# Kernel optimization log

Measured on AMD Instinct MI355X. Metric: run time of the kernel, lower is better.

## Reference

```python
import jax, jax.numpy as jnp
import numpy as np
import math

D_MODEL = 1024
NUM_HEADS = 16
D_KV = 64
INNER = NUM_HEADS * D_KV
NUM_BUCKETS = 32
MAX_DISTANCE = 128


def _relative_position_bucket(relative_position, num_buckets=NUM_BUCKETS, max_distance=MAX_DISTANCE):
    # bidirectional T5 bucketing
    n = -relative_position
    num_buckets = num_buckets // 2
    ret = (n < 0).astype(jnp.int32) * num_buckets
    n = jnp.abs(n)
    max_exact = num_buckets // 2
    is_small = n < max_exact
    n_safe = jnp.maximum(n, 1).astype(jnp.float32)  # avoid log(0); masked by is_small
    val_if_large = max_exact + (
        jnp.log(n_safe / max_exact) / math.log(max_distance / max_exact) * (num_buckets - max_exact)
    ).astype(jnp.int32)
    val_if_large = jnp.minimum(val_if_large, num_buckets - 1)
    return jnp.where(is_small, n, val_if_large) + ret


def _position_bias(rel_emb, q_len, k_len):
    ctx = jnp.arange(q_len)[:, None]
    mem = jnp.arange(k_len)[None, :]
    buckets = _relative_position_bucket(mem - ctx)          # [q, k]
    values = rel_emb[buckets]                               # [q, k, H]
    return jnp.transpose(values, (2, 0, 1))[None]           # [1, H, q, k]


def setup_inputs() -> dict:
    key = jax.random.key(0)
    ks = jax.random.split(key, 6)
    B, S = 2, 2048
    scale = 1.0 / math.sqrt(D_MODEL)
    return {
        "hidden_states": jax.random.normal(ks[0], (B, S, D_MODEL), dtype=jnp.float32),
        "mask": jnp.zeros((B, 1, 1, S), dtype=jnp.float32),
        "Wq": jax.random.normal(ks[1], (D_MODEL, INNER), dtype=jnp.float32) * scale,
        "Wk": jax.random.normal(ks[2], (D_MODEL, INNER), dtype=jnp.float32) * scale,
        "Wv": jax.random.normal(ks[3], (D_MODEL, INNER), dtype=jnp.float32) * scale,
        "Wo": jax.random.normal(ks[4], (INNER, D_MODEL), dtype=jnp.float32) * scale,
        "rel_emb": jax.random.normal(ks[5], (NUM_BUCKETS, NUM_HEADS), dtype=jnp.float32),
    }


def reference(hidden_states, mask, Wq, Wk, Wv, Wo, rel_emb):
    B, S, _ = hidden_states.shape
    def split_heads(x):
        return jnp.transpose(x.reshape(B, -1, NUM_HEADS, D_KV), (0, 2, 1, 3))  # [B,H,S,d]
    q = split_heads(hidden_states @ Wq)
    k = split_heads(hidden_states @ Wk)
    v = split_heads(hidden_states @ Wv)
    scores = jnp.einsum("bhqd,bhkd->bhqk", q, k)            # unscaled, T5-style
    position_bias = _position_bias(rel_emb, S, S)           # [1,H,S,S]
    scores = scores + position_bias + mask
    attn = jax.nn.softmax(scores, axis=-1)
    context = jnp.einsum("bhqk,bhkd->bhqd", attn, v)
    context = jnp.transpose(context, (0, 2, 1, 3)).reshape(B, S, INNER)
    output = context @ Wo
    return output, position_bias
```

## Files before the change

### kernel.cpp

```cpp
#include <hip/hip_runtime.h>
#include <cstdint>

#define AS1 __attribute__((address_space(1)))
#define AS3 __attribute__((address_space(3)))

typedef _Float16 half8 __attribute__((ext_vector_type(8)));
typedef _Float16 half4_t __attribute__((ext_vector_type(4)));
typedef float v4f __attribute__((ext_vector_type(4)));

__device__ __forceinline__ void async_ld16(const void* g, void* l) {
  __builtin_amdgcn_global_load_lds((const AS1 uint32_t*)g, (AS3 uint32_t*)l, 16, 0, 0);
}

__device__ __forceinline__ int t5_bucket(int delta) {
  int n = -delta;
  int ret = 0;
  if (n < 0) { ret = 16; n = -n; }
  if (n < 8) return n + ret;
  if (n >= 91) return 15 + ret;
  if ((n & (n - 1)) == 0) {
    int l = 31 - __clz(n);
    int v = 2 + 2 * l;
    return (v > 15 ? 15 : v) + ret;
  }
  int v = 8 + (int)(logf((float)n * 0.125f) * (8.0f / logf(16.0f)));
  return (v > 15 ? 15 : v) + ret;
}

__global__ void k_cvt(const float* __restrict__ src, _Float16* __restrict__ dst) {
  int t = blockIdx.x * 256 + threadIdx.x;
  float4 f = ((const float4*)src)[t];
  half4_t h = {(_Float16)f.x, (_Float16)f.y, (_Float16)f.z, (_Float16)f.w};
  ((half4_t*)dst)[t] = h;
}

__global__ void k_wt_all(const float* __restrict__ Wq, const float* __restrict__ Wk,
                         const float* __restrict__ Wv, const float* __restrict__ Wo,
                         _Float16* __restrict__ wqkvT, _Float16* __restrict__ woT) {
  __shared__ float tile[32][33];
  const int z = blockIdx.z;
  const float* src = (z == 0) ? Wq : (z == 1) ? Wk : (z == 2) ? Wv : Wo;
  _Float16* dst = (z < 3) ? (wqkvT + ((size_t)z << 20)) : woT;
  int tx = threadIdx.x, ty = threadIdx.y;
  int bx = blockIdx.x * 32, by = blockIdx.y * 32;
#pragma unroll
  for (int i = 0; i < 32; i += 8)
    tile[ty + i][tx] = src[(size_t)(by + ty + i) * 1024 + bx + tx];
  __syncthreads();
#pragma unroll
  for (int i = 0; i < 32; i += 8)
    dst[(size_t)(bx + ty + i) * 1024 + by + tx] = (_Float16)tile[tx][ty + i];
}

template <bool F16OUT>
__global__ __launch_bounds__(256, 2) void k_gemm(const _Float16* __restrict__ A,
                                                 const _Float16* __restrict__ BT,
                                                 void* __restrict__ Cv,
                                                 _Float16* __restrict__ vT, int K, int ldc) {
  __shared__ __align__(16) _Float16 As[128 * 32];
  __shared__ __align__(16) _Float16 Bs[128 * 32];
  const int tid = threadIdx.x;
  const int wave = tid >> 6, lane = tid & 63;
  const int l15 = lane & 15, quad = lane >> 4;
  const int m0 = blockIdx.y * 128, n0 = blockIdx.x * 128;
  const int wm = (wave >> 1) * 64, wn = (wave & 1) * 64;
  const int r0 = tid >> 2, c0 = (tid & 3) * 8;
  v4f acc[4][4] = {};
  for (int k0 = 0; k0 < K; k0 += 32) {
    __syncthreads();
    async_ld16(A + (size_t)(m0 + r0) * K + k0 + c0, (char*)As + (size_t)(wave * 64) * 16);
    async_ld16(A + (size_t)(m0 + 64 + r0) * K + k0 + c0,
               (char*)As + (size_t)(256 + wave * 64) * 16);
    async_ld16(BT + (size_t)(n0 + r0) * K + k0 + c0, (char*)Bs + (size_t)(wave * 64) * 16);
    async_ld16(BT + (size_t)(n0 + 64 + r0) * K + k0 + c0,
               (char*)Bs + (size_t)(256 + wave * 64) * 16);
    __syncthreads();
    half8 af[4], bf[4];
#pragma unroll
    for (int mt = 0; mt < 4; ++mt)
      af[mt] = *(const half8*)(As + (wm + mt * 16 + l15) * 32 + quad * 8);
#pragma unroll
    for (int nt = 0; nt < 4; ++nt)
      bf[nt] = *(const half8*)(Bs + (wn + nt * 16 + l15) * 32 + quad * 8);
#pragma unroll
    for (int mt = 0; mt < 4; ++mt)
#pragma unroll
      for (int nt = 0; nt < 4; ++nt)
        acc[mt][nt] = __builtin_amdgcn_mfma_f32_16x16x32_f16(af[mt], bf[nt], acc[mt][nt], 0, 0, 0);
  }
  if (F16OUT && n0 >= 2048) {
#pragma unroll
    for (int mt = 0; mt < 4; ++mt)
#pragma unroll
      for (int nt = 0; nt < 4; ++nt) {
        int col = n0 + wn + nt * 16 + l15 - 2048;
        int row0 = m0 + wm + mt * 16 + quad * 4;
        int bb = row0 >> 11, s0 = row0 & 2047;
        half4_t hv = {(_Float16)acc[mt][nt][0], (_Float16)acc[mt][nt][1],
                      (_Float16)acc[mt][nt][2], (_Float16)acc[mt][nt][3]};
        *(half4_t*)(vT + ((size_t)bb * 1024 + col) * 2048 + s0) = hv;
      }
    return;
  }
#pragma unroll
  for (int mt = 0; mt < 4; ++mt)
#pragma unroll
    for (int nt = 0; nt < 4; ++nt)
#pragma unroll
      for (int r = 0; r < 4; ++r) {
        int row = m0 + wm + mt * 16 + quad * 4 + r;
        int col = n0 + wn + nt * 16 + l15;
        if (F16OUT)
          ((_Float16*)Cv)[(size_t)row * ldc + col] = (_Float16)acc[mt][nt][r];
        else
          ((float*)Cv)[(size_t)row * ldc + col] = acc[mt][nt][r];
      }
}

__global__ __launch_bounds__(256, 2) void k_gemm_n64(const _Float16* __restrict__ A,
                                                     const _Float16* __restrict__ BT,
                                                     float* __restrict__ C, int K, int ldc) {
  __shared__ __align__(16) _Float16 As[128 * 32];
  __shared__ __align__(16) _Float16 Bs[64 * 32];
  const int tid = threadIdx.x;
  const int wave = tid >> 6, lane = tid & 63;
  const int l15 = lane & 15, quad = lane >> 4;
  const int m0 = blockIdx.y * 128, n0 = blockIdx.x * 64;
  const int wm = (wave >> 1) * 64, wn = (wave & 1) * 32;
  const int r0 = tid >> 2, c0 = (tid & 3) * 8;
  v4f acc[4][2] = {};
  for (int k0 = 0; k0 < K; k0 += 32) {
    __syncthreads();
    async_ld16(A + (size_t)(m0 + r0) * K + k0 + c0, (char*)As + (size_t)(wave * 64) * 16);
    async_ld16(A + (size_t)(m0 + 64 + r0) * K + k0 + c0,
               (char*)As + (size_t)(256 + wave * 64) * 16);
    async_ld16(BT + (size_t)(n0 + r0) * K + k0 + c0, (char*)Bs + (size_t)(wave * 64) * 16);
    __syncthreads();
    half8 af[4], bf[2];
#pragma unroll
    for (int mt = 0; mt < 4; ++mt)
      af[mt] = *(const half8*)(As + (wm + mt * 16 + l15) * 32 + quad * 8);
#pragma unroll
    for (int nt = 0; nt < 2; ++nt)
      bf[nt] = *(const half8*)(Bs + (wn + nt * 16 + l15) * 32 + quad * 8);
#pragma unroll
    for (int mt = 0; mt < 4; ++mt)
#pragma unroll
      for (int nt = 0; nt < 2; ++nt)
        acc[mt][nt] = __builtin_amdgcn_mfma_f32_16x16x32_f16(af[mt], bf[nt], acc[mt][nt], 0, 0, 0);
  }
#pragma unroll
  for (int mt = 0; mt < 4; ++mt)
#pragma unroll
    for (int nt = 0; nt < 2; ++nt)
#pragma unroll
      for (int r = 0; r < 4; ++r)
        C[(size_t)(m0 + wm + mt * 16 + quad * 4 + r) * ldc + n0 + wn + nt * 16 + l15] =
            acc[mt][nt][r];
}

__global__ __launch_bounds__(256, 2) void k_attn_bias(const _Float16* __restrict__ qkv,
                                                      const _Float16* __restrict__ vT,
                                                      const float* __restrict__ mask,
                                                      const float* __restrict__ rel,
                                                      _Float16* __restrict__ ctx,
                                                      float* __restrict__ outb) {
  constexpr int S = 2048, LD = 3072;
  __shared__ __align__(16) _Float16 Ks[64 * 72];
  __shared__ __align__(16) _Float16 VT[64 * 72];
  __shared__ __align__(16) _Float16 Psh[256 * 72];
  __shared__ float btab[1024];
  const int tid = threadIdx.x, wave = tid >> 6, lane = tid & 63;
  const int l15 = lane & 15, quad = lane >> 4;
  const int h = blockIdx.y, b = blockIdx.z;

  for (int j = tid; j < 1024; j += 256) btab[j] = rel[t5_bucket(j - 512) * 16 + h];
  const float c_past = rel[15 * 16 + h];
  const float c_fut = rel[31 * 16 + h];
  __syncthreads();

  if (blockIdx.x >= 8) {
    const int blk = blockIdx.x - 8;
    float4* op = (float4*)outb + (size_t)h * 2048 * 512;
#pragma unroll 4
    for (int i = 0; i < 256; ++i) {
      int idx = blk * 65536 + i * 256 + tid;
      int k4 = idx & 511;
      int q = b * 1024 + (idx >> 9);
      int kb = k4 * 4;
      float4 v;
      if (kb - q >= 91) {
        v = make_float4(c_fut, c_fut, c_fut, c_fut);
      } else if (q - kb - 3 >= 91) {
        v = make_float4(c_past, c_past, c_past, c_past);
      } else {
        v.x = btab[kb + 0 - q + 512];
        v.y = btab[kb + 1 - q + 512];
        v.z = btab[kb + 2 - q + 512];
        v.w = btab[kb + 3 - q + 512];
      }
      op[(size_t)q * 512 + k4] = v;
    }
    return;
  }

  const int q0 = blockIdx.x * 256;
  const int qbase = q0 + wave * 64;

  half8 bq[4][2];
#pragma unroll
  for (int qt = 0; qt < 4; ++qt) {
    const _Float16* qp = qkv + (size_t)(b * S + qbase + qt * 16 + l15) * LD + h * 64;
    bq[qt][0] = *(const half8*)(qp + quad * 8);
    bq[qt][1] = *(const half8*)(qp + 32 + quad * 8);
  }
  v4f o[4][4] = {};
  float mrun[4] = {-INFINITY, -INFINITY, -INFINITY, -INFINITY};
  float lrun[4] = {0.f, 0.f, 0.f, 0.f};

  const int srow = tid >> 2, scol = (tid & 3) * 8;
  const _Float16* kg = qkv + (size_t)(b * S + srow) * LD + 1024 + h * 64 + scol;
  const _Float16* vg = vT + ((size_t)((b * 16 + h) * 64 + srow)) * S + scol;
  const float4* mkp = (const float4*)(mask + (size_t)b * S);

  for (int kv0 = 0; kv0 < S; kv0 += 64) {
    half8 kr0 = *(const half8*)(kg + (size_t)kv0 * LD);
    half8 kr1 = *(const half8*)(kg + (size_t)kv0 * LD + 32);
    half8 vr0 = *(const half8*)(vg + kv0);
    half8 vr1 = *(const half8*)(vg + kv0 + 32);
    float4 mk[4];
#pragma unroll
    for (int mt = 0; mt < 4; ++mt) mk[mt] = mkp[(kv0 >> 2) + mt * 4 + quad];
    __syncthreads();
    *(half8*)(Ks + srow * 72 + scol) = kr0;
    *(half8*)(Ks + srow * 72 + scol + 32) = kr1;
    *(half8*)(VT + srow * 72 + scol) = vr0;
    *(half8*)(VT + srow * 72 + scol + 32) = vr1;
    __syncthreads();

    v4f sc[4][4] = {};
#pragma unroll
    for (int kc = 0; kc < 2; ++kc)
#pragma unroll
      for (int mt = 0; mt < 4; ++mt) {
        half8 af = *(const half8*)(Ks + (mt * 16 + l15) * 72 + kc * 32 + quad * 8);
#pragma unroll
        for (int qt = 0; qt < 4; ++qt)
          sc[qt][mt] = __builtin_amdgcn_mfma_f32_16x16x32_f16(af, bq[qt][kc], sc[qt][mt], 0, 0, 0);
      }

    const int diff = kv0 - q0;
    const bool mixed = (diff >= -153) && (diff <= 345);
    const float cf = (diff > 345) ? c_fut : c_past;
    v4f cm[4];
#pragma unroll
    for (int mt = 0; mt < 4; ++mt) {
      cm[mt][0] = mk[mt].x; cm[mt][1] = mk[mt].y; cm[mt][2] = mk[mt].z; cm[mt][3] = mk[mt].w;
      if (!mixed) {
        cm[mt][0] += cf; cm[mt][1] += cf; cm[mt][2] += cf; cm[mt][3] += cf;
      }
    }
    if (mixed) {
#pragma unroll
      for (int qt = 0; qt < 4; ++qt) {
        const int qq = qbase + qt * 16 + l15;
#pragma unroll
        for (int mt = 0; mt < 4; ++mt) {
          int base = kv0 + mt * 16 + quad * 4 - qq + 512;
#pragma unroll
          for (int r = 0; r < 4; ++r) sc[qt][mt][r] += btab[base + r] + cm[mt][r];
        }
      }
    } else {
#pragma unroll
      for (int qt = 0; qt < 4; ++qt)
#pragma unroll
        for (int mt = 0; mt < 4; ++mt)
#pragma unroll
          for (int r = 0; r < 4; ++r) sc[qt][mt][r] += cm[mt][r];
    }

#pragma unroll
    for (int qt = 0; qt < 4; ++qt) {
      v4f m4 = sc[qt][0];
#pragma unroll
      for (int r = 0; r < 4; ++r) {
        m4[r] = fmaxf(m4[r], sc[qt][1][r]);
        m4[r] = fmaxf(m4[r], sc[qt][2][r]);
        m4[r] = fmaxf(m4[r], sc[qt][3][r]);
      }
      float mx = fmaxf(fmaxf(m4[0], m4[1]), fmaxf(m4[2], m4[3]));
      mx = fmaxf(mx, __shfl_xor(mx, 16, 64));
      mx = fmaxf(mx, __shfl_xor(mx, 32, 64));
      float mnew = fmaxf(mrun[qt], mx);
      float alpha = __expf(mrun[qt] - mnew);
      mrun[qt] = mnew;
      v4f s4 = {};
#pragma unroll
      for (int mt = 0; mt < 4; ++mt)
#pragma unroll
        for (int r = 0; r < 4; ++r) {
          float p = __expf(sc[qt][mt][r] - mnew);
          sc[qt][mt][r] = p;
          s4[r] += p;
        }
      float rs = (s4[0] + s4[1]) + (s4[2] + s4[3]);
      rs += __shfl_xor(rs, 16, 64);
      rs += __shfl_xor(rs, 32, 64);
      lrun[qt] = lrun[qt] * alpha + rs;
#pragma unroll
      for (int dt = 0; dt < 4; ++dt)
#pragma unroll
        for (int r = 0; r < 4; ++r) o[qt][dt][r] *= alpha;
      const int prow = wave * 64 + qt * 16 + l15;
#pragma unroll
      for (int mt = 0; mt < 4; ++mt) {
        half4_t ph = {(_Float16)sc[qt][mt][0], (_Float16)sc[qt][mt][1],
                      (_Float16)sc[qt][mt][2], (_Float16)sc[qt][mt][3]};
        *(half4_t*)(Psh + prow * 72 + mt * 16 + quad * 4) = ph;
      }
    }

#pragma unroll
    for (int kc = 0; kc < 2; ++kc) {
      half8 av[4];
#pragma unroll
      for (int dt = 0; dt < 4; ++dt)
        av[dt] = *(const half8*)(VT + (dt * 16 + l15) * 72 + kc * 32 + quad * 8);
#pragma unroll
      for (int qt = 0; qt < 4; ++qt) {
        half8 bp = *(const half8*)(Psh + (wave * 64 + qt * 16 + l15) * 72 + kc * 32 + quad * 8);
#pragma unroll
        for (int dt = 0; dt < 4; ++dt)
          o[qt][dt] = __builtin_amdgcn_mfma_f32_16x16x32_f16(av[dt], bp, o[qt][dt], 0, 0, 0);
      }
    }
  }
#pragma unroll
  for (int qt = 0; qt < 4; ++qt) {
    float inv = 1.0f / lrun[qt];
    const size_t token = (size_t)(b * S + qbase + qt * 16 + l15);
#pragma unroll
    for (int dt = 0; dt < 4; ++dt) {
      half4_t hv = {(_Float16)(o[qt][dt][0] * inv), (_Float16)(o[qt][dt][1] * inv),
                    (_Float16)(o[qt][dt][2] * inv), (_Float16)(o[qt][dt][3] * inv)};
      *(half4_t*)(ctx + token * 1024 + h * 64 + dt * 16 + quad * 4) = hv;
    }
  }
}

extern "C" void kernel_launch(void* const* d_in, const int* in_sizes, int n_in,
                              void* d_out, int out_size, void* d_ws, size_t ws_size,
                              hipStream_t stream) {
  const float* hs = (const float*)d_in[0];
  const float* mask = (const float*)d_in[1];
  const float* Wq = (const float*)d_in[2];
  const float* Wk = (const float*)d_in[3];
  const float* Wv = (const float*)d_in[4];
  const float* Wo = (const float*)d_in[5];
  const float* rel = (const float*)d_in[6];
  float* out = (float*)d_out;

  char* ws = (char*)d_ws;
  _Float16* hsF = (_Float16*)(ws);
  _Float16* wqkvT = (_Float16*)(ws + (8u << 20));
  _Float16* woT = (_Float16*)(ws + (14u << 20));
  _Float16* qkv = (_Float16*)(ws + (16u << 20));
  _Float16* ctx = (_Float16*)(ws + (40u << 20));
  _Float16* vT = (_Float16*)(ws + (48u << 20));

  k_cvt<<<4096, 256, 0, stream>>>(hs, hsF);
  k_wt_all<<<dim3(32, 32, 4), dim3(32, 8), 0, stream>>>(Wq, Wk, Wv, Wo, wqkvT, woT);

  k_gemm<true><<<dim3(24, 32), 256, 0, stream>>>(hsF, wqkvT, qkv, vT, 1024, 3072);
  k_attn_bias<<<dim3(16, 16, 2), 256, 0, stream>>>(qkv, vT, mask, rel, ctx, out + 4194304);
  k_gemm_n64<<<dim3(16, 32), 256, 0, stream>>>(ctx, woT, out, 1024, 1024);
}
```

Before: 483.0 us.

## Interleave position-bias writes into the attention KV loop instead of separate blocks

```diff
diff --git a/kernel.cpp b/kernel.cpp
--- a/kernel.cpp
+++ b/kernel.cpp
@@ -159,7 +159,7 @@
             acc[mt][nt][r];
 }
 
-__global__ __launch_bounds__(256, 2) void k_attn_bias(const _Float16* __restrict__ qkv,
+__global__ __launch_bounds__(256, 1) void k_attn_bias(const _Float16* __restrict__ qkv,
                                                       const _Float16* __restrict__ vT,
                                                       const float* __restrict__ mask,
                                                       const float* __restrict__ rel,
@@ -179,31 +179,6 @@
   const float c_fut = rel[31 * 16 + h];
   __syncthreads();
 
-  if (blockIdx.x >= 8) {
-    const int blk = blockIdx.x - 8;
-    float4* op = (float4*)outb + (size_t)h * 2048 * 512;
-#pragma unroll 4
-    for (int i = 0; i < 256; ++i) {
-      int idx = blk * 65536 + i * 256 + tid;
-      int k4 = idx & 511;
-      int q = b * 1024 + (idx >> 9);
-      int kb = k4 * 4;
-      float4 v;
-      if (kb - q >= 91) {
-        v = make_float4(c_fut, c_fut, c_fut, c_fut);
-      } else if (q - kb - 3 >= 91) {
-        v = make_float4(c_past, c_past, c_past, c_past);
-      } else {
-        v.x = btab[kb + 0 - q + 512];
-        v.y = btab[kb + 1 - q + 512];
-        v.z = btab[kb + 2 - q + 512];
-        v.w = btab[kb + 3 - q + 512];
-      }
-      op[(size_t)q * 512 + k4] = v;
-    }
-    return;
-  }
-
   const int q0 = blockIdx.x * 256;
   const int qbase = q0 + wave * 64;
 
@@ -222,8 +197,12 @@
   const _Float16* kg = qkv + (size_t)(b * S + srow) * LD + 1024 + h * 64 + scol;
   const _Float16* vg = vT + ((size_t)((b * 16 + h) * 64 + srow)) * S + scol;
   const float4* mkp = (const float4*)(mask + (size_t)b * S);
+  float4* const obase = (float4*)outb + (size_t)h * 2048 * 512;
+  const int brow = tid >> 5;
+  const int bcol0 = tid & 31;
 
   for (int kv0 = 0; kv0 < S; kv0 += 64) {
+    const int iter = kv0 >> 6;
     half8 kr0 = *(const half8*)(kg + (size_t)kv0 * LD);
     half8 kr1 = *(const half8*)(kg + (size_t)kv0 * LD + 32);
     half8 vr0 = *(const half8*)(vg + kv0);
@@ -237,6 +216,28 @@
     *(half8*)(VT + srow * 72 + scol) = vr0;
     *(half8*)(VT + srow * 72 + scol + 32) = vr1;
     __syncthreads();
+
+    {
+      const int qr = q0 + iter * 8 + brow;
+      float4* orow = obase + (size_t)qr * 512 + b * 256;
+#pragma unroll
+      for (int j = 0; j < 8; ++j) {
+        int c4 = bcol0 + j * 32;
+        int kb = (b * 256 + c4) * 4;
+        float4 v;
+        if (kb - qr >= 91) {
+          v = make_float4(c_fut, c_fut, c_fut, c_fut);
+        } else if (qr - kb - 3 >= 91) {
+          v = make_float4(c_past, c_past, c_past, c_past);
+        } else {
+          v.x = btab[kb + 0 - qr + 512];
+          v.y = btab[kb + 1 - qr + 512];
+          v.z = btab[kb + 2 - qr + 512];
+          v.w = btab[kb + 3 - qr + 512];
+        }
+        orow[c4] = v;
+      }
+    }
 
     v4f sc[4][4] = {};
 #pragma unroll
@@ -373,6 +374,6 @@
   k_wt_all<<<dim3(32, 32, 4), dim3(32, 8), 0, stream>>>(Wq, Wk, Wv, Wo, wqkvT, woT);
 
   k_gemm<true><<<dim3(24, 32), 256, 0, stream>>>(hsF, wqkvT, qkv, vT, 1024, 3072);
-  k_attn_bias<<<dim3(16, 16, 2), 256, 0, stream>>>(qkv, vT, mask, rel, ctx, out + 4194304);
+  k_attn_bias<<<dim3(8, 16, 2), 256, 0, stream>>>(qkv, vT, mask, rel, ctx, out + 4194304);
   k_gemm_n64<<<dim3(16, 32), 256, 0, stream>>>(ctx, woT, out, 1024, 1024);
 }
```

Measured after the change: 455.9 us. 5.6% less time.
